# Kernel tuning notes

Hardware: AMD Instinct MI355X
Metric: run time of the kernel (lower is better)

Reference implementation:

```python
import jax, jax.numpy as jnp
import numpy as np

B, H, L, D = 2, 16, 2048, 64


def setup_inputs() -> dict:
    key = jax.random.key(0)
    kq, kk, kv = jax.random.split(key, 3)
    return {
        "query": jax.random.normal(kq, (B, H, L, D), dtype=jnp.float32),
        "key": jax.random.normal(kk, (B, H, L, D), dtype=jnp.float32),
        "value": jax.random.normal(kv, (B, H, L, D), dtype=jnp.float32),
        "dhead": D,
        "causal": 1,
    }


def reference(query, key, value, dhead, causal):
    # mode='dhead': muP attention with scale 1/dhead (not 1/sqrt(dhead)).
    # Inputs/outputs in [B, H, L, D] layout (the torch code transposes to
    # [B, L, H, D] for the einsum and transposes back; net layout is the same).
    scale = 1.0 / dhead
    a = jnp.einsum('bhld,bhLd->bhlL', query, key) * scale  # [B,H,L,L]
    if causal:
        seq = a.shape[-1]
        mask = jnp.tril(jnp.ones((seq, seq), dtype=bool))  # [L,L]
        a = jnp.where(mask, a, jnp.float32(-jnp.inf))
    a = jax.nn.softmax(a, axis=-1)
    out = jnp.einsum('bhlL,bhLd->bhld', a, value)  # [B,H,L,D]
    return out
```

## Files before the change

### kernel.cpp

```cpp
#include <hip/hip_runtime.h>

#define BHH 32
#define SEQ 2048
#define DH 64
#define BK 64
#define NKT (SEQ / BK)
#define NT  (BHH * NKT)

typedef __attribute__((ext_vector_type(8))) _Float16 half8_t;
typedef __attribute__((ext_vector_type(4))) _Float16 half4_t;
typedef __attribute__((ext_vector_type(2))) _Float16 half2_t;
typedef __attribute__((ext_vector_type(4))) float f32x4;

__device__ __forceinline__ void async_copy16(const void* g, const void* lds) {
    __builtin_amdgcn_global_load_lds(
        (const __attribute__((address_space(1))) unsigned int*)g,
        (__attribute__((address_space(3))) unsigned int*)lds, 16, 0, 0);
}

__device__ __forceinline__ half2_t pkrtz(float a, float b) {
    return __builtin_bit_cast(half2_t, __builtin_amdgcn_cvt_pkrtz(a, b));
}

__global__ __launch_bounds__(256) void prep_kv(const float* __restrict__ K,
                                               const float* __restrict__ V,
                                               _Float16* __restrict__ Kf,
                                               _Float16* __restrict__ Vf) {
    __shared__ _Float16 l[64 * 76];
    const int t = threadIdx.x;
    const int wave = t >> 6, lane = t & 63, ln15 = lane & 15, quad = lane >> 4;
    const int row = t >> 2, col0 = (t & 3) * 16;
    int b = blockIdx.x;

    if (b < NT) {
        const float4* src = (const float4*)(K + (size_t)b * 4096 + row * 64 + col0);
        #pragma unroll
        for (int q = 0; q < 2; ++q) {
            float4 f0 = src[q * 2], f1 = src[q * 2 + 1];
            half8_t w = { (_Float16)f0.x, (_Float16)f0.y, (_Float16)f0.z, (_Float16)f0.w,
                          (_Float16)f1.x, (_Float16)f1.y, (_Float16)f1.z, (_Float16)f1.w };
            *(half8_t*)&l[row * 72 + col0 + q * 8] = w;
        }
        __syncthreads();
        #pragma unroll
        for (int p = 0; p < 2; ++p) {
            const int bid = wave * 2 + p, c = bid >> 1, k0 = bid & 1;
            half8_t w = *(const half8_t*)&l[(c * 16 + ln15) * 72 + k0 * 32 + quad * 8];
            *(half8_t*)&Kf[(size_t)b * 4096 + bid * 512 + lane * 8] = w;
        }
    } else {
        b -= NT;
        const float4* src = (const float4*)(V + (size_t)b * 4096 + row * 64 + col0);
        #pragma unroll
        for (int q = 0; q < 4; ++q) {
            float4 f = src[q];
            half4_t w = { (_Float16)f.x, (_Float16)f.y, (_Float16)f.z, (_Float16)f.w };
            *(half4_t*)&l[row * 76 + col0 + q * 4] = w;
        }
        __syncthreads();
        #pragma unroll
        for (int p = 0; p < 2; ++p) {
            const int f = wave * 2 + p, cn = f >> 1, k1 = f & 1;
            half8_t w;
            #pragma unroll
            for (int jj = 0; jj < 8; ++jj) {
                const int krow = k1 * 32 + ((jj & 4) << 2) + quad * 4 + (jj & 3);
                w[jj] = l[krow * 76 + cn * 16 + ln15];
            }
            *(half8_t*)&Vf[(size_t)b * 4096 + f * 512 + lane * 8] = w;
        }
    }
}

__global__ __launch_bounds__(128, 2) void fattn_kernel(
        const float* __restrict__ Q, const _Float16* __restrict__ Kf,
        const _Float16* __restrict__ Vf, float* __restrict__ O) {
    const int bh = blockIdx.x & 31;
    const int pr = blockIdx.x >> 5;
    const int tid  = threadIdx.x;
    const int wave = tid >> 6;
    const int lane = tid & 63;
    const int ln15 = lane & 15;
    const int quad = lane >> 4;

    __shared__ _Float16 ldsK[2][4096];
    __shared__ _Float16 ldsV[2][4096];

    const size_t base = (size_t)bh * SEQ * DH;
    const size_t tb = (size_t)(bh * NKT) * 4096;

    const _Float16* gsrc = (wave ? Vf : Kf) + tb + lane * 8;
    _Float16* dst0 = (wave ? &ldsV[0][0] : &ldsK[0][0]);
    _Float16* dst1 = (wave ? &ldsV[1][0] : &ldsK[1][0]);

    #define STAGE(kt_, dd_) do {                                         \
        const _Float16* s_ = gsrc + (size_t)(kt_) * 4096;                \
        _Float16* d_ = (dd_);                                            \
        _Pragma("unroll")                                                \
        for (int f_ = 0; f_ < 8; ++f_)                                   \
            async_copy16(s_ + f_ * 512, d_ + f_ * 512);                  \
    } while (0)

    const _Float16* kbase = &ldsK[0][0] + lane * 8;
    const _Float16* vbase = &ldsV[0][0] + lane * 8;
    const int kq4 = quad * 4;
    const float qscale = 1.44269504f / 64.0f;

    union P8 { half2_t h2[4]; half8_t h8; };

    #pragma unroll 1
    for (int pass = 0; pass < 2; ++pass) {
        const int q32  = pass ? (63 - pr) : pr;
        const int qb64 = q32 >> 1;
        const int nkt  = qb64 + 1;
        const int qrow = q32 * 32 + wave * 16;
        const int relrow = (q32 & 1) * 32 + wave * 16 + ln15;

        if (pass)
            asm volatile("s_barrier" ::: "memory");

        STAGE(0, dst0);

        half8_t qfrag[2];
        {
            const float* qp = Q + base + (size_t)(qrow + ln15) * DH + quad * 8;
            #pragma unroll
            for (int k0 = 0; k0 < 2; ++k0) {
                float4 a = *(const float4*)(qp + k0 * 32);
                float4 b2 = *(const float4*)(qp + k0 * 32 + 4);
                qfrag[k0] = (half8_t){
                    (_Float16)(a.x * qscale), (_Float16)(a.y * qscale),
                    (_Float16)(a.z * qscale), (_Float16)(a.w * qscale),
                    (_Float16)(b2.x * qscale), (_Float16)(b2.y * qscale),
                    (_Float16)(b2.z * qscale), (_Float16)(b2.w * qscale) };
            }
        }
        asm volatile("s_waitcnt vmcnt(0) lgkmcnt(0)\n\ts_barrier" ::: "memory");

        f32x4 acc[4] = {};
        float l_lane = 0.f;

        for (int kt = 0; kt < nkt; ++kt) {
            const _Float16* kk = kbase + (kt & 1) * 4096;
            const _Float16* vv = vbase + (kt & 1) * 4096;
            if (kt + 1 < nkt) STAGE(kt + 1, (kt & 1) ? dst0 : dst1);

            f32x4 st[4];
            #pragma unroll
            for (int c = 0; c < 4; ++c) {
                half8_t kf0 = *(const half8_t*)(kk + c * 1024);
                half8_t kf1 = *(const half8_t*)(kk + c * 1024 + 512);
                f32x4 a = {};
                a = __builtin_amdgcn_mfma_f32_16x16x32_f16(kf0, qfrag[0], a, 0, 0, 0);
                a = __builtin_amdgcn_mfma_f32_16x16x32_f16(kf1, qfrag[1], a, 0, 0, 0);
                st[c] = a;
            }

            float p[4][4];
            #pragma unroll
            for (int c = 0; c < 4; ++c)
                #pragma unroll
                for (int rr = 0; rr < 4; ++rr)
                    p[c][rr] = __builtin_amdgcn_exp2f(st[c][rr]);

            if (kt == qb64) {
                #pragma unroll
                for (int c = 0; c < 4; ++c)
                    #pragma unroll
                    for (int rr = 0; rr < 4; ++rr)
                        if (c * 16 + kq4 + rr > relrow) p[c][rr] = 0.f;
            }

            float s0 = (p[0][0] + p[0][1]) + (p[0][2] + p[0][3]);
            float s1 = (p[1][0] + p[1][1]) + (p[1][2] + p[1][3]);
            float s2 = (p[2][0] + p[2][1]) + (p[2][2] + p[2][3]);
            float s3 = (p[3][0] + p[3][1]) + (p[3][2] + p[3][3]);
            l_lane += (s0 + s1) + (s2 + s3);

            P8 u0, u1;
            u0.h2[0] = pkrtz(p[0][0], p[0][1]);
            u0.h2[1] = pkrtz(p[0][2], p[0][3]);
            u0.h2[2] = pkrtz(p[1][0], p[1][1]);
            u0.h2[3] = pkrtz(p[1][2], p[1][3]);
            u1.h2[0] = pkrtz(p[2][0], p[2][1]);
            u1.h2[1] = pkrtz(p[2][2], p[2][3]);
            u1.h2[2] = pkrtz(p[3][0], p[3][1]);
            u1.h2[3] = pkrtz(p[3][2], p[3][3]);
            half8_t pb0 = u0.h8, pb1 = u1.h8;

            #pragma unroll
            for (int cn = 0; cn < 4; ++cn) {
                half8_t vf0 = *(const half8_t*)(vv + cn * 1024);
                acc[cn] = __builtin_amdgcn_mfma_f32_16x16x32_f16(vf0, pb0, acc[cn], 0, 0, 0);
                half8_t vf1 = *(const half8_t*)(vv + cn * 1024 + 512);
                acc[cn] = __builtin_amdgcn_mfma_f32_16x16x32_f16(vf1, pb1, acc[cn], 0, 0, 0);
            }

            asm volatile("s_waitcnt vmcnt(0) lgkmcnt(0)\n\ts_barrier" ::: "memory");
        }

        {
            float l_i = l_lane + __shfl_xor(l_lane, 16);
            l_i += __shfl_xor(l_i, 32);
            const float rl = 1.0f / l_i;
            float* op = O + base + (size_t)(qrow + ln15) * DH;
            #pragma unroll
            for (int cn = 0; cn < 4; ++cn) {
                float4 o;
                o.x = acc[cn][0] * rl;
                o.y = acc[cn][1] * rl;
                o.z = acc[cn][2] * rl;
                o.w = acc[cn][3] * rl;
                *(float4*)(op + cn * 16 + kq4) = o;
            }
        }
    }
    #undef STAGE
}

extern "C" void kernel_launch(void* const* d_in, const int* in_sizes, int n_in,
                              void* d_out, int out_size, void* d_ws, size_t ws_size,
                              hipStream_t stream) {
    const float* Q = (const float*)d_in[0];
    const float* K = (const float*)d_in[1];
    const float* V = (const float*)d_in[2];
    float* O = (float*)d_out;
    _Float16* Kf = (_Float16*)d_ws;
    _Float16* Vf = Kf + (size_t)NT * 4096;
    prep_kv<<<2 * NT, 256, 0, stream>>>(K, V, Kf, Vf);
    fattn_kernel<<<1024, 128, 0, stream>>>(Q, Kf, Vf, O);
}
```

Before: 126.6 us.

## Split long causal query blocks across two workgroups with partial-sum reduction

Replaces the paired-query-block scheme, where 128-thread blocks ran two 32-row passes, with 256-thread blocks each handling one 64-row query block. The 24 longest query blocks per head have their KV range split in half across two workgroups. Those write unnormalized partial outputs and row sums to workspace, and a new reduce kernel combines and normalizes them. This aims to balance causal work and raise occupancy, at the cost of an extra kernel launch and partial-buffer traffic. The softmax skips max subtraction, so partial sums add linearly.

New measurement: 129.8 us. +2.5%, slower.

```diff
diff --git a/kernel.cpp b/kernel.cpp
--- a/kernel.cpp
+++ b/kernel.cpp
@@ -6,6 +6,9 @@
 #define BK 64
 #define NKT (SEQ / BK)
 #define NT  (BHH * NKT)
+
+#define OP_STRIDE 4194304u
+#define LP_STRIDE 65536u
 
 typedef __attribute__((ext_vector_type(8))) _Float16 half8_t;
 typedef __attribute__((ext_vector_type(4))) _Float16 half4_t;
@@ -72,11 +75,29 @@
     }
 }
 
-__global__ __launch_bounds__(128, 2) void fattn_kernel(
+__global__ __launch_bounds__(256, 5) void fattn_kernel(
         const float* __restrict__ Q, const _Float16* __restrict__ Kf,
-        const _Float16* __restrict__ Vf, float* __restrict__ O) {
+        const _Float16* __restrict__ Vf, float* __restrict__ O,
+        float* __restrict__ Opart, float* __restrict__ lpart) {
+    const int g  = blockIdx.x >> 5;
     const int bh = blockIdx.x & 31;
-    const int pr = blockIdx.x >> 5;
+    int qb, k0, k1, slot;
+    bool do_partial;
+    if (g < 48) {
+        qb = 31 - (g >> 1);
+        slot = g & 1;
+        const int h = (qb + 2) >> 1;
+        k0 = slot ? h : 0;
+        k1 = slot ? qb + 1 : h;
+        do_partial = true;
+    } else {
+        qb = 55 - g;
+        slot = 0;
+        k0 = 0;
+        k1 = qb + 1;
+        do_partial = false;
+    }
+
     const int tid  = threadIdx.x;
     const int wave = tid >> 6;
     const int lane = tid & 63;
@@ -87,123 +108,117 @@
     __shared__ _Float16 ldsV[2][4096];
 
     const size_t base = (size_t)bh * SEQ * DH;
+    const int qrow = qb * 64 + wave * 16;
     const size_t tb = (size_t)(bh * NKT) * 4096;
 
-    const _Float16* gsrc = (wave ? Vf : Kf) + tb + lane * 8;
-    _Float16* dst0 = (wave ? &ldsV[0][0] : &ldsK[0][0]);
-    _Float16* dst1 = (wave ? &ldsV[1][0] : &ldsK[1][0]);
+    const _Float16* gsrc = ((wave < 2) ? Kf : Vf) + tb + (wave & 1) * 2048 + lane * 8;
+    _Float16* dst0 = ((wave < 2) ? &ldsK[0][0] : &ldsV[0][0]) + (wave & 1) * 2048;
+    _Float16* dst1 = ((wave < 2) ? &ldsK[1][0] : &ldsV[1][0]) + (wave & 1) * 2048;
 
     #define STAGE(kt_, dd_) do {                                         \
         const _Float16* s_ = gsrc + (size_t)(kt_) * 4096;                \
         _Float16* d_ = (dd_);                                            \
-        _Pragma("unroll")                                                \
-        for (int f_ = 0; f_ < 8; ++f_)                                   \
-            async_copy16(s_ + f_ * 512, d_ + f_ * 512);                  \
+        async_copy16(s_,        d_);                                     \
+        async_copy16(s_ + 512,  d_ + 512);                               \
+        async_copy16(s_ + 1024, d_ + 1024);                              \
+        async_copy16(s_ + 1536, d_ + 1536);                              \
     } while (0)
+
+    STAGE(k0, (k0 & 1) ? dst1 : dst0);
+
+    const float qscale = 1.44269504f / 64.0f;
+    half8_t qfrag[2];
+    {
+        const float* qp = Q + base + (size_t)(qrow + ln15) * DH + quad * 8;
+        #pragma unroll
+        for (int c0 = 0; c0 < 2; ++c0) {
+            float4 a = *(const float4*)(qp + c0 * 32);
+            float4 b2 = *(const float4*)(qp + c0 * 32 + 4);
+            qfrag[c0] = (half8_t){
+                (_Float16)(a.x * qscale), (_Float16)(a.y * qscale),
+                (_Float16)(a.z * qscale), (_Float16)(a.w * qscale),
+                (_Float16)(b2.x * qscale), (_Float16)(b2.y * qscale),
+                (_Float16)(b2.z * qscale), (_Float16)(b2.w * qscale) };
+        }
+    }
+    asm volatile("s_waitcnt vmcnt(0) lgkmcnt(0)\n\ts_barrier" ::: "memory");
+
+    f32x4 acc[4] = {};
+    float l_lane = 0.f;
 
     const _Float16* kbase = &ldsK[0][0] + lane * 8;
     const _Float16* vbase = &ldsV[0][0] + lane * 8;
+    const int myrel = wave * 16 + ln15;
     const int kq4 = quad * 4;
-    const float qscale = 1.44269504f / 64.0f;
 
     union P8 { half2_t h2[4]; half8_t h8; };
 
-    #pragma unroll 1
-    for (int pass = 0; pass < 2; ++pass) {
-        const int q32  = pass ? (63 - pr) : pr;
-        const int qb64 = q32 >> 1;
-        const int nkt  = qb64 + 1;
-        const int qrow = q32 * 32 + wave * 16;
-        const int relrow = (q32 & 1) * 32 + wave * 16 + ln15;
-
-        if (pass)
-            asm volatile("s_barrier" ::: "memory");
-
-        STAGE(0, dst0);
-
-        half8_t qfrag[2];
-        {
-            const float* qp = Q + base + (size_t)(qrow + ln15) * DH + quad * 8;
-            #pragma unroll
-            for (int k0 = 0; k0 < 2; ++k0) {
-                float4 a = *(const float4*)(qp + k0 * 32);
-                float4 b2 = *(const float4*)(qp + k0 * 32 + 4);
-                qfrag[k0] = (half8_t){
-                    (_Float16)(a.x * qscale), (_Float16)(a.y * qscale),
-                    (_Float16)(a.z * qscale), (_Float16)(a.w * qscale),
-                    (_Float16)(b2.x * qscale), (_Float16)(b2.y * qscale),
-                    (_Float16)(b2.z * qscale), (_Float16)(b2.w * qscale) };
-            }
-        }
-        asm volatile("s_waitcnt vmcnt(0) lgkmcnt(0)\n\ts_barrier" ::: "memory");
-
-        f32x4 acc[4] = {};
-        float l_lane = 0.f;
-
-        for (int kt = 0; kt < nkt; ++kt) {
-            const _Float16* kk = kbase + (kt & 1) * 4096;
-            const _Float16* vv = vbase + (kt & 1) * 4096;
-            if (kt + 1 < nkt) STAGE(kt + 1, (kt & 1) ? dst0 : dst1);
-
-            f32x4 st[4];
-            #pragma unroll
-            for (int c = 0; c < 4; ++c) {
-                half8_t kf0 = *(const half8_t*)(kk + c * 1024);
-                half8_t kf1 = *(const half8_t*)(kk + c * 1024 + 512);
-                f32x4 a = {};
-                a = __builtin_amdgcn_mfma_f32_16x16x32_f16(kf0, qfrag[0], a, 0, 0, 0);
-                a = __builtin_amdgcn_mfma_f32_16x16x32_f16(kf1, qfrag[1], a, 0, 0, 0);
-                st[c] = a;
-            }
-
-            float p[4][4];
+    for (int kt = k0; kt < k1; ++kt) {
+        const _Float16* kk = kbase + (kt & 1) * 4096;
+        const _Float16* vv = vbase + (kt & 1) * 4096;
+        if (kt + 1 < k1) STAGE(kt + 1, ((kt + 1) & 1) ? dst1 : dst0);
+
+        f32x4 st[4];
+        #pragma unroll
+        for (int c = 0; c < 4; ++c) {
+            half8_t kf0 = *(const half8_t*)(kk + c * 1024);
+            half8_t kf1 = *(const half8_t*)(kk + c * 1024 + 512);
+            f32x4 a = {};
+            a = __builtin_amdgcn_mfma_f32_16x16x32_f16(kf0, qfrag[0], a, 0, 0, 0);
+            a = __builtin_amdgcn_mfma_f32_16x16x32_f16(kf1, qfrag[1], a, 0, 0, 0);
+            st[c] = a;
+        }
+
+        float p[4][4];
+        #pragma unroll
+        for (int c = 0; c < 4; ++c)
+            #pragma unroll
+            for (int rr = 0; rr < 4; ++rr)
+                p[c][rr] = __builtin_amdgcn_exp2f(st[c][rr]);
+
+        if (kt == qb) {
             #pragma unroll
             for (int c = 0; c < 4; ++c)
                 #pragma unroll
                 for (int rr = 0; rr < 4; ++rr)
-                    p[c][rr] = __builtin_amdgcn_exp2f(st[c][rr]);
-
-            if (kt == qb64) {
-                #pragma unroll
-                for (int c = 0; c < 4; ++c)
-                    #pragma unroll
-                    for (int rr = 0; rr < 4; ++rr)
-                        if (c * 16 + kq4 + rr > relrow) p[c][rr] = 0.f;
-            }
-
-            float s0 = (p[0][0] + p[0][1]) + (p[0][2] + p[0][3]);
-            float s1 = (p[1][0] + p[1][1]) + (p[1][2] + p[1][3]);
-            float s2 = (p[2][0] + p[2][1]) + (p[2][2] + p[2][3]);
-            float s3 = (p[3][0] + p[3][1]) + (p[3][2] + p[3][3]);
-            l_lane += (s0 + s1) + (s2 + s3);
-
-            P8 u0, u1;
-            u0.h2[0] = pkrtz(p[0][0], p[0][1]);
-            u0.h2[1] = pkrtz(p[0][2], p[0][3]);
-            u0.h2[2] = pkrtz(p[1][0], p[1][1]);
-            u0.h2[3] = pkrtz(p[1][2], p[1][3]);
-            u1.h2[0] = pkrtz(p[2][0], p[2][1]);
-            u1.h2[1] = pkrtz(p[2][2], p[2][3]);
-            u1.h2[2] = pkrtz(p[3][0], p[3][1]);
-            u1.h2[3] = pkrtz(p[3][2], p[3][3]);
-            half8_t pb0 = u0.h8, pb1 = u1.h8;
-
-            #pragma unroll
-            for (int cn = 0; cn < 4; ++cn) {
-                half8_t vf0 = *(const half8_t*)(vv + cn * 1024);
-                acc[cn] = __builtin_amdgcn_mfma_f32_16x16x32_f16(vf0, pb0, acc[cn], 0, 0, 0);
-                half8_t vf1 = *(const half8_t*)(vv + cn * 1024 + 512);
-                acc[cn] = __builtin_amdgcn_mfma_f32_16x16x32_f16(vf1, pb1, acc[cn], 0, 0, 0);
-            }
-
-            asm volatile("s_waitcnt vmcnt(0) lgkmcnt(0)\n\ts_barrier" ::: "memory");
-        }
-
-        {
-            float l_i = l_lane + __shfl_xor(l_lane, 16);
-            l_i += __shfl_xor(l_i, 32);
+                    if (c * 16 + kq4 + rr > myrel) p[c][rr] = 0.f;
+        }
+
+        float s0 = (p[0][0] + p[0][1]) + (p[0][2] + p[0][3]);
+        float s1 = (p[1][0] + p[1][1]) + (p[1][2] + p[1][3]);
+        float s2 = (p[2][0] + p[2][1]) + (p[2][2] + p[2][3]);
+        float s3 = (p[3][0] + p[3][1]) + (p[3][2] + p[3][3]);
+        l_lane += (s0 + s1) + (s2 + s3);
+
+        P8 u0, u1;
+        u0.h2[0] = pkrtz(p[0][0], p[0][1]);
+        u0.h2[1] = pkrtz(p[0][2], p[0][3]);
+        u0.h2[2] = pkrtz(p[1][0], p[1][1]);
+        u0.h2[3] = pkrtz(p[1][2], p[1][3]);
+        u1.h2[0] = pkrtz(p[2][0], p[2][1]);
+        u1.h2[1] = pkrtz(p[2][2], p[2][3]);
+        u1.h2[2] = pkrtz(p[3][0], p[3][1]);
+        u1.h2[3] = pkrtz(p[3][2], p[3][3]);
+        half8_t pb0 = u0.h8, pb1 = u1.h8;
+
+        #pragma unroll
+        for (int cn = 0; cn < 4; ++cn) {
+            half8_t vf0 = *(const half8_t*)(vv + cn * 1024);
+            acc[cn] = __builtin_amdgcn_mfma_f32_16x16x32_f16(vf0, pb0, acc[cn], 0, 0, 0);
+            half8_t vf1 = *(const half8_t*)(vv + cn * 1024 + 512);
+            acc[cn] = __builtin_amdgcn_mfma_f32_16x16x32_f16(vf1, pb1, acc[cn], 0, 0, 0);
+        }
+
+        asm volatile("s_waitcnt vmcnt(0) lgkmcnt(0)\n\ts_barrier" ::: "memory");
+    }
+
+    {
+        float l_i = l_lane + __shfl_xor(l_lane, 16);
+        l_i += __shfl_xor(l_i, 32);
+        const int row = qrow + ln15;
+        if (!do_partial) {
             const float rl = 1.0f / l_i;
-            float* op = O + base + (size_t)(qrow + ln15) * DH;
+            float* op = O + base + (size_t)row * DH;
             #pragma unroll
             for (int cn = 0; cn < 4; ++cn) {
                 float4 o;
@@ -213,9 +228,49 @@
                 o.w = acc[cn][3] * rl;
                 *(float4*)(op + cn * 16 + kq4) = o;
             }
+        } else {
+            float* pb = Opart + (size_t)slot * OP_STRIDE
+                      + ((size_t)bh * SEQ + row) * DH;
+            #pragma unroll
+            for (int cn = 0; cn < 4; ++cn) {
+                float4 o;
+                o.x = acc[cn][0];
+                o.y = acc[cn][1];
+                o.z = acc[cn][2];
+                o.w = acc[cn][3];
+                *(float4*)(pb + cn * 16 + kq4) = o;
+            }
+            if (quad == 0)
+                lpart[slot * LP_STRIDE + bh * SEQ + row] = l_i;
         }
     }
     #undef STAGE
+}
+
+#define RED_TOTAL (32 * 1536 * 16)
+__global__ __launch_bounds__(256) void reduce_kernel(
+        const float* __restrict__ Opart, const float* __restrict__ lpart,
+        float* __restrict__ O) {
+    int i = blockIdx.x * 256 + threadIdx.x;
+    #pragma unroll 1
+    for (; i < RED_TOTAL; i += 768 * 256) {
+        const int bh  = i / (1536 * 16);
+        const int r   = i - bh * (1536 * 16);
+        const int row = 512 + (r >> 4);
+        const int c4  = (r & 15) << 2;
+        const size_t off = ((size_t)bh * SEQ + row) * DH + c4;
+        float4 a = *(const float4*)(Opart + off);
+        float4 b = *(const float4*)(Opart + OP_STRIDE + off);
+        const float l0 = lpart[bh * SEQ + row];
+        const float l1 = lpart[LP_STRIDE + bh * SEQ + row];
+        const float rl = 1.0f / (l0 + l1);
+        float4 o;
+        o.x = (a.x + b.x) * rl;
+        o.y = (a.y + b.y) * rl;
+        o.z = (a.z + b.z) * rl;
+        o.w = (a.w + b.w) * rl;
+        *(float4*)(O + off) = o;
+    }
 }
 
 extern "C" void kernel_launch(void* const* d_in, const int* in_sizes, int n_in,
@@ -227,6 +282,9 @@
     float* O = (float*)d_out;
     _Float16* Kf = (_Float16*)d_ws;
     _Float16* Vf = Kf + (size_t)NT * 4096;
+    float* Opart = (float*)d_ws + 4 * 1024 * 1024;
+    float* lpart = Opart + 2 * (size_t)OP_STRIDE;
     prep_kv<<<2 * NT, 256, 0, stream>>>(K, V, Kf, Vf);
-    fattn_kernel<<<1024, 128, 0, stream>>>(Q, Kf, Vf, O);
-}
+    fattn_kernel<<<56 * BHH, 256, 0, stream>>>(Q, Kf, Vf, O, Opart, lpart);
+    reduce_kernel<<<768, 256, 0, stream>>>(Opart, lpart, O);
+}
```

## Use 128-row query tiles with 4 waves, two row-blocks per wave

Applied to the files above, without the earlier changes.

Replaces the paired-pass 32-row blocks (2 waves) with 128-row query tiles processed by 4 waves, each handling two 16-row sub-blocks that share every K/V fragment read from LDS. Blocks are ordered heaviest-first to balance the causal workload, and each wave now stages a quarter of the K/V tile. This aims to halve LDS reads per MFMA and cut the number of K/V tile loads per query row. In exchange it raises register pressure, since the accumulators and Q fragments are doubled, and the grid drops to 512 larger blocks, which reduces parallelism and wastes more work on the diagonal tiles.

Result: faster. 123.6 us (-2.4%).

```diff
diff --git a/kernel.cpp b/kernel.cpp
--- a/kernel.cpp
+++ b/kernel.cpp
@@ -72,11 +72,12 @@
     }
 }
 
-__global__ __launch_bounds__(128, 2) void fattn_kernel(
+__global__ __launch_bounds__(256, 3) void fattn_kernel(
         const float* __restrict__ Q, const _Float16* __restrict__ Kf,
         const _Float16* __restrict__ Vf, float* __restrict__ O) {
     const int bh = blockIdx.x & 31;
-    const int pr = blockIdx.x >> 5;
+    const int qb = 15 - (blockIdx.x >> 5);
+    const int nkt = 2 * qb + 2;
     const int tid  = threadIdx.x;
     const int wave = tid >> 6;
     const int lane = tid & 63;
@@ -87,132 +88,169 @@
     __shared__ _Float16 ldsV[2][4096];
 
     const size_t base = (size_t)bh * SEQ * DH;
+    const int qrow = qb * 128 + wave * 32;
     const size_t tb = (size_t)(bh * NKT) * 4096;
 
-    const _Float16* gsrc = (wave ? Vf : Kf) + tb + lane * 8;
-    _Float16* dst0 = (wave ? &ldsV[0][0] : &ldsK[0][0]);
-    _Float16* dst1 = (wave ? &ldsV[1][0] : &ldsK[1][0]);
+    const _Float16* gsrc = ((wave < 2) ? Kf : Vf) + tb + (wave & 1) * 2048 + lane * 8;
+    _Float16* dst0 = ((wave < 2) ? &ldsK[0][0] : &ldsV[0][0]) + (wave & 1) * 2048;
+    _Float16* dst1 = ((wave < 2) ? &ldsK[1][0] : &ldsV[1][0]) + (wave & 1) * 2048;
 
     #define STAGE(kt_, dd_) do {                                         \
         const _Float16* s_ = gsrc + (size_t)(kt_) * 4096;                \
         _Float16* d_ = (dd_);                                            \
-        _Pragma("unroll")                                                \
-        for (int f_ = 0; f_ < 8; ++f_)                                   \
-            async_copy16(s_ + f_ * 512, d_ + f_ * 512);                  \
+        async_copy16(s_,        d_);                                     \
+        async_copy16(s_ + 512,  d_ + 512);                               \
+        async_copy16(s_ + 1024, d_ + 1024);                              \
+        async_copy16(s_ + 1536, d_ + 1536);                              \
     } while (0)
+
+    STAGE(0, dst0);
+
+    const float qscale = 1.44269504f / 64.0f;
+    half8_t qfA[2], qfB[2];
+    {
+        const float* qpA = Q + base + (size_t)(qrow + ln15) * DH + quad * 8;
+        const float* qpB = qpA + 16 * DH;
+        #pragma unroll
+        for (int k0 = 0; k0 < 2; ++k0) {
+            float4 a = *(const float4*)(qpA + k0 * 32);
+            float4 b2 = *(const float4*)(qpA + k0 * 32 + 4);
+            qfA[k0] = (half8_t){
+                (_Float16)(a.x * qscale), (_Float16)(a.y * qscale),
+                (_Float16)(a.z * qscale), (_Float16)(a.w * qscale),
+                (_Float16)(b2.x * qscale), (_Float16)(b2.y * qscale),
+                (_Float16)(b2.z * qscale), (_Float16)(b2.w * qscale) };
+            float4 c = *(const float4*)(qpB + k0 * 32);
+            float4 d2 = *(const float4*)(qpB + k0 * 32 + 4);
+            qfB[k0] = (half8_t){
+                (_Float16)(c.x * qscale), (_Float16)(c.y * qscale),
+                (_Float16)(c.z * qscale), (_Float16)(c.w * qscale),
+                (_Float16)(d2.x * qscale), (_Float16)(d2.y * qscale),
+                (_Float16)(d2.z * qscale), (_Float16)(d2.w * qscale) };
+        }
+    }
+    asm volatile("s_waitcnt vmcnt(0) lgkmcnt(0)\n\ts_barrier" ::: "memory");
+
+    f32x4 accA[4] = {}, accB[4] = {};
+    float lA_lane = 0.f, lB_lane = 0.f;
 
     const _Float16* kbase = &ldsK[0][0] + lane * 8;
     const _Float16* vbase = &ldsV[0][0] + lane * 8;
+    const int rowA = qrow + ln15;
     const int kq4 = quad * 4;
-    const float qscale = 1.44269504f / 64.0f;
+    const int ktdiag = 2 * qb;
 
     union P8 { half2_t h2[4]; half8_t h8; };
 
-    #pragma unroll 1
-    for (int pass = 0; pass < 2; ++pass) {
-        const int q32  = pass ? (63 - pr) : pr;
-        const int qb64 = q32 >> 1;
-        const int nkt  = qb64 + 1;
-        const int qrow = q32 * 32 + wave * 16;
-        const int relrow = (q32 & 1) * 32 + wave * 16 + ln15;
-
-        if (pass)
-            asm volatile("s_barrier" ::: "memory");
-
-        STAGE(0, dst0);
-
-        half8_t qfrag[2];
-        {
-            const float* qp = Q + base + (size_t)(qrow + ln15) * DH + quad * 8;
+    for (int kt = 0; kt < nkt; ++kt) {
+        const _Float16* kk = kbase + (kt & 1) * 4096;
+        const _Float16* vv = vbase + (kt & 1) * 4096;
+        if (kt + 1 < nkt) STAGE(kt + 1, ((kt + 1) & 1) ? dst1 : dst0);
+
+        f32x4 stA[4], stB[4];
+        #pragma unroll
+        for (int c = 0; c < 4; ++c) {
+            half8_t kf0 = *(const half8_t*)(kk + c * 1024);
+            half8_t kf1 = *(const half8_t*)(kk + c * 1024 + 512);
+            f32x4 a = {};
+            a = __builtin_amdgcn_mfma_f32_16x16x32_f16(kf0, qfA[0], a, 0, 0, 0);
+            a = __builtin_amdgcn_mfma_f32_16x16x32_f16(kf1, qfA[1], a, 0, 0, 0);
+            stA[c] = a;
+            f32x4 b = {};
+            b = __builtin_amdgcn_mfma_f32_16x16x32_f16(kf0, qfB[0], b, 0, 0, 0);
+            b = __builtin_amdgcn_mfma_f32_16x16x32_f16(kf1, qfB[1], b, 0, 0, 0);
+            stB[c] = b;
+        }
+
+        float pA[4][4], pB[4][4];
+        #pragma unroll
+        for (int c = 0; c < 4; ++c)
             #pragma unroll
-            for (int k0 = 0; k0 < 2; ++k0) {
-                float4 a = *(const float4*)(qp + k0 * 32);
-                float4 b2 = *(const float4*)(qp + k0 * 32 + 4);
-                qfrag[k0] = (half8_t){
-                    (_Float16)(a.x * qscale), (_Float16)(a.y * qscale),
-                    (_Float16)(a.z * qscale), (_Float16)(a.w * qscale),
-                    (_Float16)(b2.x * qscale), (_Float16)(b2.y * qscale),
-                    (_Float16)(b2.z * qscale), (_Float16)(b2.w * qscale) };
+            for (int rr = 0; rr < 4; ++rr) {
+                pA[c][rr] = __builtin_amdgcn_exp2f(stA[c][rr]);
+                pB[c][rr] = __builtin_amdgcn_exp2f(stB[c][rr]);
             }
-        }
-        asm volatile("s_waitcnt vmcnt(0) lgkmcnt(0)\n\ts_barrier" ::: "memory");
-
-        f32x4 acc[4] = {};
-        float l_lane = 0.f;
-
-        for (int kt = 0; kt < nkt; ++kt) {
-            const _Float16* kk = kbase + (kt & 1) * 4096;
-            const _Float16* vv = vbase + (kt & 1) * 4096;
-            if (kt + 1 < nkt) STAGE(kt + 1, (kt & 1) ? dst0 : dst1);
-
-            f32x4 st[4];
-            #pragma unroll
-            for (int c = 0; c < 4; ++c) {
-                half8_t kf0 = *(const half8_t*)(kk + c * 1024);
-                half8_t kf1 = *(const half8_t*)(kk + c * 1024 + 512);
-                f32x4 a = {};
-                a = __builtin_amdgcn_mfma_f32_16x16x32_f16(kf0, qfrag[0], a, 0, 0, 0);
-                a = __builtin_amdgcn_mfma_f32_16x16x32_f16(kf1, qfrag[1], a, 0, 0, 0);
-                st[c] = a;
-            }
-
-            float p[4][4];
+
+        if (kt >= ktdiag) {
+            const int kb = kt * 64;
             #pragma unroll
             for (int c = 0; c < 4; ++c)
                 #pragma unroll
-                for (int rr = 0; rr < 4; ++rr)
-                    p[c][rr] = __builtin_amdgcn_exp2f(st[c][rr]);
-
-            if (kt == qb64) {
-                #pragma unroll
-                for (int c = 0; c < 4; ++c)
-                    #pragma unroll
-                    for (int rr = 0; rr < 4; ++rr)
-                        if (c * 16 + kq4 + rr > relrow) p[c][rr] = 0.f;
-            }
-
-            float s0 = (p[0][0] + p[0][1]) + (p[0][2] + p[0][3]);
-            float s1 = (p[1][0] + p[1][1]) + (p[1][2] + p[1][3]);
-            float s2 = (p[2][0] + p[2][1]) + (p[2][2] + p[2][3]);
-            float s3 = (p[3][0] + p[3][1]) + (p[3][2] + p[3][3]);
-            l_lane += (s0 + s1) + (s2 + s3);
-
-            P8 u0, u1;
-            u0.h2[0] = pkrtz(p[0][0], p[0][1]);
-            u0.h2[1] = pkrtz(p[0][2], p[0][3]);
-            u0.h2[2] = pkrtz(p[1][0], p[1][1]);
-            u0.h2[3] = pkrtz(p[1][2], p[1][3]);
-            u1.h2[0] = pkrtz(p[2][0], p[2][1]);
-            u1.h2[1] = pkrtz(p[2][2], p[2][3]);
-            u1.h2[2] = pkrtz(p[3][0], p[3][1]);
-            u1.h2[3] = pkrtz(p[3][2], p[3][3]);
-            half8_t pb0 = u0.h8, pb1 = u1.h8;
-
-            #pragma unroll
-            for (int cn = 0; cn < 4; ++cn) {
-                half8_t vf0 = *(const half8_t*)(vv + cn * 1024);
-                acc[cn] = __builtin_amdgcn_mfma_f32_16x16x32_f16(vf0, pb0, acc[cn], 0, 0, 0);
-                half8_t vf1 = *(const half8_t*)(vv + cn * 1024 + 512);
-                acc[cn] = __builtin_amdgcn_mfma_f32_16x16x32_f16(vf1, pb1, acc[cn], 0, 0, 0);
-            }
-
-            asm volatile("s_waitcnt vmcnt(0) lgkmcnt(0)\n\ts_barrier" ::: "memory");
+                for (int rr = 0; rr < 4; ++rr) {
+                    const int kabs = kb + c * 16 + kq4 + rr;
+                    if (kabs > rowA)      pA[c][rr] = 0.f;
+                    if (kabs > rowA + 16) pB[c][rr] = 0.f;
+                }
         }
 
         {
-            float l_i = l_lane + __shfl_xor(l_lane, 16);
-            l_i += __shfl_xor(l_i, 32);
-            const float rl = 1.0f / l_i;
-            float* op = O + base + (size_t)(qrow + ln15) * DH;
-            #pragma unroll
-            for (int cn = 0; cn < 4; ++cn) {
-                float4 o;
-                o.x = acc[cn][0] * rl;
-                o.y = acc[cn][1] * rl;
-                o.z = acc[cn][2] * rl;
-                o.w = acc[cn][3] * rl;
-                *(float4*)(op + cn * 16 + kq4) = o;
-            }
+            float s0 = (pA[0][0] + pA[0][1]) + (pA[0][2] + pA[0][3]);
+            float s1 = (pA[1][0] + pA[1][1]) + (pA[1][2] + pA[1][3]);
+            float s2 = (pA[2][0] + pA[2][1]) + (pA[2][2] + pA[2][3]);
+            float s3 = (pA[3][0] + pA[3][1]) + (pA[3][2] + pA[3][3]);
+            lA_lane += (s0 + s1) + (s2 + s3);
+            float t0 = (pB[0][0] + pB[0][1]) + (pB[0][2] + pB[0][3]);
+            float t1 = (pB[1][0] + pB[1][1]) + (pB[1][2] + pB[1][3]);
+            float t2 = (pB[2][0] + pB[2][1]) + (pB[2][2] + pB[2][3]);
+            float t3 = (pB[3][0] + pB[3][1]) + (pB[3][2] + pB[3][3]);
+            lB_lane += (t0 + t1) + (t2 + t3);
+        }
+
+        P8 uA0, uA1, uB0, uB1;
+        uA0.h2[0] = pkrtz(pA[0][0], pA[0][1]);
+        uA0.h2[1] = pkrtz(pA[0][2], pA[0][3]);
+        uA0.h2[2] = pkrtz(pA[1][0], pA[1][1]);
+        uA0.h2[3] = pkrtz(pA[1][2], pA[1][3]);
+        uA1.h2[0] = pkrtz(pA[2][0], pA[2][1]);
+        uA1.h2[1] = pkrtz(pA[2][2], pA[2][3]);
+        uA1.h2[2] = pkrtz(pA[3][0], pA[3][1]);
+        uA1.h2[3] = pkrtz(pA[3][2], pA[3][3]);
+        uB0.h2[0] = pkrtz(pB[0][0], pB[0][1]);
+        uB0.h2[1] = pkrtz(pB[0][2], pB[0][3]);
+        uB0.h2[2] = pkrtz(pB[1][0], pB[1][1]);
+        uB0.h2[3] = pkrtz(pB[1][2], pB[1][3]);
+        uB1.h2[0] = pkrtz(pB[2][0], pB[2][1]);
+        uB1.h2[1] = pkrtz(pB[2][2], pB[2][3]);
+        uB1.h2[2] = pkrtz(pB[3][0], pB[3][1]);
+        uB1.h2[3] = pkrtz(pB[3][2], pB[3][3]);
+        half8_t pbA0 = uA0.h8, pbA1 = uA1.h8, pbB0 = uB0.h8, pbB1 = uB1.h8;
+
+        #pragma unroll
+        for (int cn = 0; cn < 4; ++cn) {
+            half8_t vf0 = *(const half8_t*)(vv + cn * 1024);
+            half8_t vf1 = *(const half8_t*)(vv + cn * 1024 + 512);
+            accA[cn] = __builtin_amdgcn_mfma_f32_16x16x32_f16(vf0, pbA0, accA[cn], 0, 0, 0);
+            accA[cn] = __builtin_amdgcn_mfma_f32_16x16x32_f16(vf1, pbA1, accA[cn], 0, 0, 0);
+            accB[cn] = __builtin_amdgcn_mfma_f32_16x16x32_f16(vf0, pbB0, accB[cn], 0, 0, 0);
+            accB[cn] = __builtin_amdgcn_mfma_f32_16x16x32_f16(vf1, pbB1, accB[cn], 0, 0, 0);
+        }
+
+        asm volatile("s_waitcnt vmcnt(0) lgkmcnt(0)\n\ts_barrier" ::: "memory");
+    }
+
+    {
+        float lA = lA_lane + __shfl_xor(lA_lane, 16);
+        lA += __shfl_xor(lA, 32);
+        float lB = lB_lane + __shfl_xor(lB_lane, 16);
+        lB += __shfl_xor(lB, 32);
+        const float rlA = 1.0f / lA;
+        const float rlB = 1.0f / lB;
+        float* opA = O + base + (size_t)rowA * DH;
+        float* opB = opA + 16 * DH;
+        #pragma unroll
+        for (int cn = 0; cn < 4; ++cn) {
+            float4 oa;
+            oa.x = accA[cn][0] * rlA;
+            oa.y = accA[cn][1] * rlA;
+            oa.z = accA[cn][2] * rlA;
+            oa.w = accA[cn][3] * rlA;
+            *(float4*)(opA + cn * 16 + kq4) = oa;
+            float4 ob;
+            ob.x = accB[cn][0] * rlB;
+            ob.y = accB[cn][1] * rlB;
+            ob.z = accB[cn][2] * rlB;
+            ob.w = accB[cn][3] * rlB;
+            *(float4*)(opB + cn * 16 + kq4) = ob;
         }
     }
     #undef STAGE
@@ -228,5 +266,5 @@
     _Float16* Kf = (_Float16*)d_ws;
     _Float16* Vf = Kf + (size_t)NT * 4096;
     prep_kv<<<2 * NT, 256, 0, stream>>>(K, V, Kf, Vf);
-    fattn_kernel<<<1024, 128, 0, stream>>>(Q, Kf, Vf, O);
-}
+    fattn_kernel<<<16 * BHH, 256, 0, stream>>>(Q, Kf, Vf, O);
+}
```
